# Optimization experiments

Hardware: AMD Instinct MI355X
Metric: run time of the kernel (lower is better)

The kernel has to match this reference:

```python
import jax, jax.numpy as jnp
import numpy as np

N, E, D = 20000, 160000, 128   # nodes, edges, d_model
GH, HC = 4, 128                # TransformerConv heads, per-head channels (= out_channels)
MH = 4                         # temporal MHA heads
MC = D // MH                   # temporal MHA per-head dim
EPS = 1e-5


def layer_norm(x, g, b):
    mu = x.mean(-1, keepdims=True)
    var = ((x - mu) ** 2).mean(-1, keepdims=True)
    return (x - mu) * jax.lax.rsqrt(var + EPS) * g + b


def forward(x, temporal_encoding, gq_w, gq_b, gk_w, gk_b, gv_w, gv_b, gs_w, gs_b,
            mha_wq, mha_bq, mha_wk, mha_bk, mha_wv, mha_bv, mha_wo, mha_bo,
            ffn_w1, ffn_b1, ffn_w2, ffn_b2,
            ln1_g, ln1_b, ln2_g, ln2_b, ln3_g, ln3_b, edge_index):
    src, dst = edge_index[0], edge_index[1]
    n = x.shape[0]
    # --- TransformerConv(in=D, out=D, heads=GH, concat=False, root_weight=True) ---
    q = (x @ gq_w.T + gq_b).reshape(n, GH, HC)
    k = (x @ gk_w.T + gk_b).reshape(n, GH, HC)
    v = (x @ gv_w.T + gv_b).reshape(n, GH, HC)
    # per-edge attention logits: <q_i, k_j> / sqrt(out_channels), message j->i
    alpha = (q[dst] * k[src]).sum(-1) / jnp.sqrt(jnp.asarray(HC, x.dtype))  # [E, GH]
    # numerically-stable segment softmax over incoming edges of each dst node
    m = jax.ops.segment_max(alpha, dst, num_segments=n)                     # [N, GH]
    ex = jnp.exp(alpha - m[dst])
    den = jax.ops.segment_sum(ex, dst, num_segments=n)
    w = ex / den[dst]                                                       # [E, GH]
    agg = jax.ops.segment_sum(w[..., None] * v[src], dst, num_segments=n)  # [N, GH, HC]
    graph_out = agg.mean(1) + (x @ gs_w.T + gs_b)  # concat=False -> head mean; + root skip lin
    x1 = layer_norm(x + graph_out, ln1_g, ln1_b)   # dropout is identity at eval
    # --- temporal MHA: per-node query (len 1) attends to its temporal encoding (kv len 1) ---
    tq = (x1 @ mha_wq.T + mha_bq).reshape(n, MH, MC)
    tk = (temporal_encoding @ mha_wk.T + mha_bk).reshape(n, MH, MC)
    tv = (temporal_encoding @ mha_wv.T + mha_bv).reshape(n, MH, MC)
    scores = (tq * tk).sum(-1, keepdims=True) / jnp.sqrt(jnp.asarray(MC, x.dtype))  # [N, MH, 1]
    attn = jax.nn.softmax(scores, axis=-1)  # exactly ones (single kv position); kept for fidelity
    temp_out = (attn * tv).reshape(n, D) @ mha_wo.T + mha_bo
    x2 = layer_norm(x1 + temp_out, ln2_g, ln2_b)
    # --- FFN ---
    h = jax.nn.relu(x2 @ ffn_w1.T + ffn_b1)
    ffn_out = h @ ffn_w2.T + ffn_b2
    return layer_norm(x2 + ffn_out, ln3_g, ln3_b)


def setup_inputs() -> dict:
    ks = jax.random.split(jax.random.key(0), 16)
    s = 0.05
    def p(i, shape):
        return jax.random.normal(ks[i], shape, jnp.float32) * s
    z = lambda *sh: jnp.zeros(sh, jnp.float32)
    o = lambda *sh: jnp.ones(sh, jnp.float32)
    return {
        "x": p(0, (N, D)),
        "temporal_encoding": p(1, (N, D)),
        "gq_w": p(2, (GH * HC, D)), "gq_b": z(GH * HC),
        "gk_w": p(3, (GH * HC, D)), "gk_b": z(GH * HC),
        "gv_w": p(4, (GH * HC, D)), "gv_b": z(GH * HC),
        "gs_w": p(5, (D, D)), "gs_b": z(D),
        "mha_wq": p(6, (D, D)), "mha_bq": z(D),
        "mha_wk": p(7, (D, D)), "mha_bk": z(D),
        "mha_wv": p(8, (D, D)), "mha_bv": z(D),
        "mha_wo": p(9, (D, D)), "mha_bo": z(D),
        "ffn_w1": p(10, (4 * D, D)), "ffn_b1": z(4 * D),
        "ffn_w2": p(11, (D, 4 * D)), "ffn_b2": z(D),
        "ln1_g": o(D), "ln1_b": z(D),
        "ln2_g": o(D), "ln2_b": z(D),
        "ln3_g": o(D), "ln3_b": z(D),
        "edge_index": jax.random.randint(ks[12], (2, E), 0, N, jnp.int32),
    }


def reference(x, temporal_encoding, gq_w, gq_b, gk_w, gk_b, gv_w, gv_b, gs_w, gs_b,
              mha_wq, mha_bq, mha_wk, mha_bk, mha_wv, mha_bv, mha_wo, mha_bo,
              ffn_w1, ffn_b1, ffn_w2, ffn_b2,
              ln1_g, ln1_b, ln2_g, ln2_b, ln3_g, ln3_b, edge_index):
    return forward(x, temporal_encoding, gq_w, gq_b, gk_w, gk_b, gv_w, gv_b, gs_w, gs_b,
                   mha_wq, mha_bq, mha_wk, mha_bk, mha_wv, mha_bv, mha_wo, mha_bo,
                   ffn_w1, ffn_b1, ffn_w2, ffn_b2,
                   ln1_g, ln1_b, ln2_g, ln2_b, ln3_g, ln3_b, edge_index)
```

## Files before the change

### kernel.cpp

```cpp
#include <hip/hip_runtime.h>

#define NN 20000
#define EE 160000
#define DD 128
#define GHC 512
#define INV_SQRT_HC 0.08838834764831845f

typedef __attribute__((ext_vector_type(8))) short short8;
typedef __attribute__((ext_vector_type(4))) short short4v;
typedef __attribute__((ext_vector_type(4))) float float4v;
typedef __attribute__((ext_vector_type(2))) float float2v;
typedef __attribute__((ext_vector_type(4))) unsigned uint4v;
typedef __attribute__((ext_vector_type(2))) unsigned uint2v;

__device__ inline float bf2f(unsigned short u) {
    union { unsigned u; float f; } x; x.u = ((unsigned)u) << 16; return x.f;
}
__device__ inline unsigned short f2bf(float f) {
    union { float f; unsigned u; } x; x.f = f;
    unsigned u = x.u;
    unsigned r = (u + 0x7fffu + ((u >> 16) & 1u)) >> 16;
    return (unsigned short)r;
}
__device__ inline unsigned cvt_pk_bf16(float a, float b) {
    unsigned d;
    asm("v_cvt_pk_bf16_f32 %0, %1, %2" : "=v"(d) : "v"(a), "v"(b));
    return d;
}

__device__ inline void stage16(const short8* gsrc, short8* ldst) {
    __builtin_amdgcn_global_load_lds(
        (const __attribute__((address_space(1))) void*)gsrc,
        (__attribute__((address_space(3))) void*)ldst, 16, 0, 0);
}

#if defined(__has_builtin)
#if __has_builtin(__builtin_amdgcn_cvt_pk_f32_fp8) && __has_builtin(__builtin_amdgcn_cvt_pk_fp8_f32)
#define HW_FP8 1
#endif
#endif
#ifndef HW_FP8
#define HW_FP8 0
#endif

#if !HW_FP8
__device__ inline unsigned char sw_enc_fp8(float f) {
    if (!(f == f)) return 0x7f;
    unsigned s = (f < 0.f) ? 0x80u : 0u;
    float a = fabsf(f);
    if (a >= 448.f) return (unsigned char)(s | 0x7e);
    if (a < 5.96046448e-8f) return (unsigned char)s;
    int e; frexpf(a, &e);
    int E = e - 1;
    if (E < -6) E = -6;
    float q = ldexpf(rintf(ldexpf(a, 3 - E)), E - 3);
    if (q == 0.f) return (unsigned char)s;
    union { float f; unsigned u; } x; x.f = q;
    int qe = (int)((x.u >> 23) & 0xff) - 127;
    if (qe < -6) {
        unsigned mant = (unsigned)rintf(ldexpf(q, 9));
        return (unsigned char)(s | mant);
    }
    unsigned mant = (x.u >> 20) & 7;
    int ebits = qe + 7;
    if (ebits > 15) { ebits = 15; mant = 6; }
    return (unsigned char)(s | ((unsigned)ebits << 3) | mant);
}
__device__ inline float sw_dec_fp8(unsigned char u) {
    unsigned s = u >> 7, e = (u >> 3) & 15, m = u & 7;
    float v = e ? ldexpf((float)(8 + m), (int)e - 10) : ldexpf((float)m, -9);
    return s ? -v : v;
}
#endif

__device__ inline unsigned fp8_enc4(float a, float b, float c, float d) {
#if HW_FP8
    int r = __builtin_amdgcn_cvt_pk_fp8_f32(a, b, 0, false);
    r = __builtin_amdgcn_cvt_pk_fp8_f32(c, d, r, true);
    return (unsigned)r;
#else
    return (unsigned)sw_enc_fp8(a) | ((unsigned)sw_enc_fp8(b) << 8)
         | ((unsigned)sw_enc_fp8(c) << 16) | ((unsigned)sw_enc_fp8(d) << 24);
#endif
}
__device__ inline float2v fp8_dec2_lo(unsigned w) {
#if HW_FP8
    return __builtin_amdgcn_cvt_pk_f32_fp8((int)w, false);
#else
    float2v r;
    r[0] = sw_dec_fp8((unsigned char)(w & 0xff));
    r[1] = sw_dec_fp8((unsigned char)((w >> 8) & 0xff));
    return r;
#endif
}
__device__ inline float2v fp8_dec2_hi(unsigned w) {
#if HW_FP8
    return __builtin_amdgcn_cvt_pk_f32_fp8((int)w, true);
#else
    float2v r;
    r[0] = sw_dec_fp8((unsigned char)((w >> 16) & 0xff));
    r[1] = sw_dec_fp8((unsigned char)(w >> 24));
    return r;
#endif
}

struct WPack { const void* in[18]; };
__device__ __constant__ const int WSZ[18] = {
    65536, 65536, 65536, 512, 512, 512,
    16384, 128, 65536, 512, 65536, 128,
    128, 128, 128, 128, 128, 128 };

__global__ void prep_kernel(const float* __restrict__ x, const float* __restrict__ te,
                            unsigned short* __restrict__ xcout, WPack p,
                            unsigned short* __restrict__ wcout,
                            const float* __restrict__ wv, const float* __restrict__ bv,
                            const float* __restrict__ wo, const float* __restrict__ bo,
                            unsigned short* __restrict__ wcomb,
                            unsigned short* __restrict__ bcomb,
                            const int* __restrict__ e_dst, int* __restrict__ counts)
{
    const int b = blockIdx.x;
    const int tid = threadIdx.x;
    if (b < 1024) {
        const long n4half = (long)NN * DD / 4;
        short4v* out4 = reinterpret_cast<short4v*>(xcout);
        long i = (long)b * 256 + tid;
        const long stride = 1024L * 256;
        const long tot = 2 * n4half;
        for (; i < tot; i += stride) {
            const float4v* src = (i < n4half)
                ? reinterpret_cast<const float4v*>(x)
                : reinterpret_cast<const float4v*>(te) - n4half;
            float4v v = src[i];
            short4v o;
            o[0] = (short)f2bf(v[0]); o[1] = (short)f2bf(v[1]);
            o[2] = (short)f2bf(v[2]); o[3] = (short)f2bf(v[3]);
            out4[i] = o;
        }
    } else if (b < 1600) {
        const int seg = (b - 1024) >> 5;
        const int rep = (b - 1024) & 31;
        int off = 0;
#pragma unroll
        for (int s = 0; s < 18; ++s) if (s < seg) off += WSZ[s];
        const int n = WSZ[seg];
        const float* q = (const float*)p.in[seg];
        for (int i = rep * 256 + tid; i < n; i += 32 * 256)
            wcout[off + i] = f2bf(q[i]);
    } else if (b < 1664) {
        int e = (b - 1600) * 256 + tid;
        int i = e >> 7, kk = e & 127;
        float s = 0.f;
        for (int j = 0; j < 128; ++j)
            s += wo[i * 128 + j] * wv[j * 128 + kk];
        wcomb[e] = f2bf(s);
        if (b == 1600 && tid < 128) {
            float t = 0.f;
            for (int j = 0; j < 128; ++j) t += wo[tid * 128 + j] * bv[j];
            bcomb[tid] = f2bf(t + bo[tid]);
        }
    } else {
        int e = (b - 1664) * 256 + tid;
        if (e < EE) {
            int d = e_dst[e];
            if (d >= 0 && d < NN) atomicAdd(&counts[d], 1);
        }
    }
}

__global__ __launch_bounds__(256) void gemm3_kernel(
    const unsigned short* __restrict__ A, const unsigned short* __restrict__ W,
    const unsigned short* __restrict__ bias, unsigned short* __restrict__ out,
    unsigned char* __restrict__ kvout, int M, int Nout, int split, int relu,
    int nxg, int ncol)
{
    __shared__ short8 wslab[2048];
    __shared__ __attribute__((aligned(16))) unsigned stile4[4][16][32];
    const int tid  = threadIdx.x;
    const int lane = tid & 63;
    const int wid  = tid >> 6;
    const int quad = lane >> 4;
    const int l15  = lane & 15;

    const int nb  = nxg * ncol;
    const int qq  = nb >> 3, rm = nb & 7;
    const int xcd = blockIdx.x & 7, slot = blockIdx.x >> 3;
    const int c   = (xcd < rm) ? xcd * (qq + 1) + slot
                               : rm * (qq + 1) + (xcd - rm) * qq + slot;
    const int xg = c / ncol;
    const int yg = c - xg * ncol;
    const int colbase0 = yg * 128;
    const int rowg = xg * 256;

    const bool isfp8 = (colbase0 >= split);
    const int kvcol = colbase0 - split;
    const int which = isfp8 ? (kvcol >> 9) : 0;
    const int head  = isfp8 ? ((kvcol & 511) >> 7) : 0;

    const short8* A8 = reinterpret_cast<const short8*>(A);
    const short8* W8 = reinterpret_cast<const short8*>(W);

    short8 a4[4];
    {
        int arow = rowg + wid * 16 + l15;
        if (arow >= M) arow = M - 1;
#pragma unroll
        for (int i = 0; i < 4; ++i) a4[i] = A8[(size_t)arow * 16 + i * 4 + quad];
    }

#pragma unroll
    for (int rep = 0; rep < 8; ++rep) {
        const int fi  = (rep * 4 + wid) & 3;
        const int ft  = rep & 3;
        const int ftt = rep >> 2;
        const int wrow = colbase0 + ftt * 64 + 16 * ft + l15;
        stage16(&W8[(size_t)wrow * 16 + fi * 4 + quad], &wslab[rep * 256 + wid * 64]);
    }

    short4v bs4[2][4];
#pragma unroll
    for (int tt = 0; tt < 2; ++tt)
#pragma unroll
        for (int t = 0; t < 4; ++t)
            bs4[tt][t] = *reinterpret_cast<const short4v*>(
                &bias[colbase0 + tt * 64 + 16 * t + quad * 4]);

    __syncthreads();

    unsigned* fpd = &stile4[wid][0][0];

#pragma unroll
    for (int tg = 0; tg < 4; ++tg) {
        const int rowbase = rowg + tg * 64 + wid * 16;

        short8 a4n[4];
        if (tg < 3) {
            int arow = rowbase + 64 + l15;
            if (arow >= M) arow = M - 1;
#pragma unroll
            for (int i = 0; i < 4; ++i) a4n[i] = A8[(size_t)arow * 16 + i * 4 + quad];
        }

#pragma unroll
        for (int tt = 0; tt < 2; ++tt) {
            float4v acc[4];
#pragma unroll
            for (int t = 0; t < 4; ++t) acc[t] = (float4v){0.f, 0.f, 0.f, 0.f};

#pragma unroll
            for (int i = 0; i < 4; ++i) {
#pragma unroll
                for (int t = 0; t < 4; ++t) {
                    short8 wb = wslab[((tt * 4 + t) * 4 + i) * 64 + lane];
                    acc[t] = __builtin_amdgcn_mfma_f32_16x16x32_bf16(wb, a4[i], acc[t], 0, 0, 0);
                }
            }

            if (!isfp8) {
#pragma unroll
                for (int t = 0; t < 4; ++t) {
                    float v0 = acc[t][0] + bf2f((unsigned short)bs4[tt][t][0]);
                    float v1 = acc[t][1] + bf2f((unsigned short)bs4[tt][t][1]);
                    float v2 = acc[t][2] + bf2f((unsigned short)bs4[tt][t][2]);
                    float v3 = acc[t][3] + bf2f((unsigned short)bs4[tt][t][3]);
                    if (relu) {
                        v0 = fmaxf(v0, 0.f); v1 = fmaxf(v1, 0.f);
                        v2 = fmaxf(v2, 0.f); v3 = fmaxf(v3, 0.f);
                    }
                    uint2v d = { cvt_pk_bf16(v0, v1), cvt_pk_bf16(v2, v3) };
                    const int dc = (8 * t + quad * 2) ^ ((l15 & 7) << 2);
                    *reinterpret_cast<uint2v*>(&stile4[wid][l15][dc]) = d;
                }
                const int rr0 = lane >> 3;
                const int cd  = (lane & 7) * 4;
#pragma unroll
                for (int it = 0; it < 2; ++it) {
                    int rw = rr0 + it * 8;
                    int grow = rowbase + rw;
                    if (grow < M) {
                        const int cs = cd ^ ((rw & 7) << 2);
                        uint4v v = *reinterpret_cast<const uint4v*>(&stile4[wid][rw][cs]);
                        *reinterpret_cast<uint4v*>(&out[(size_t)grow * Nout + colbase0 + tt * 64 + cd * 2]) = v;
                    }
                }
            } else {
#pragma unroll
                for (int t = 0; t < 4; ++t) {
                    float v0 = (acc[t][0] + bf2f((unsigned short)bs4[tt][t][0])) * 256.f;
                    float v1 = (acc[t][1] + bf2f((unsigned short)bs4[tt][t][1])) * 256.f;
                    float v2 = (acc[t][2] + bf2f((unsigned short)bs4[tt][t][2])) * 256.f;
                    float v3 = (acc[t][3] + bf2f((unsigned short)bs4[tt][t][3])) * 256.f;
                    const int dc = (tt * 16 + 4 * t + quad) ^ ((l15 & 7) << 2);
                    fpd[l15 * 32 + dc] = fp8_enc4(v0, v1, v2, v3);
                }
            }
        }

        if (isfp8) {
#pragma unroll
            for (int it = 0; it < 2; ++it) {
                int u = lane + it * 64;
                int row = u >> 3;
                int part = u & 7;
                int grow = rowbase + row;
                if (grow < M) {
                    const int db = row * 32 + ((part * 4) ^ ((row & 7) << 2));
                    uint4v v = *reinterpret_cast<const uint4v*>(&fpd[db]);
                    size_t ro = (size_t)grow * 1024 + (size_t)which * 512
                              + (size_t)head * 128 + (size_t)part * 16;
                    *reinterpret_cast<uint4v*>(kvout + ro) = v;
                }
            }
        }

        if (tg < 3) {
#pragma unroll
            for (int i = 0; i < 4; ++i) a4[i] = a4n[i];
        }
    }
}

__global__ __launch_bounds__(256) void tail_kernel(
    const unsigned short* __restrict__ A1, const unsigned short* __restrict__ W1g,
    const unsigned short* __restrict__ b1g,
    const unsigned short* __restrict__ A2, const unsigned short* __restrict__ W2g,
    const unsigned short* __restrict__ b2g,
    const float* __restrict__ rx, const float* __restrict__ ragg,
    const unsigned short* __restrict__ g1, const unsigned short* __restrict__ be1,
    const unsigned short* __restrict__ g2, const unsigned short* __restrict__ be2,
    const unsigned short* __restrict__ fw1, const unsigned short* __restrict__ fb1,
    const unsigned short* __restrict__ fw2, const unsigned short* __restrict__ fb2,
    const unsigned short* __restrict__ g3, const unsigned short* __restrict__ be3,
    float* __restrict__ outf, int M)
{
    __shared__ short8 wslab[2048];
    __shared__ __attribute__((aligned(16))) unsigned short htile[64 * 128];
    const int tid  = threadIdx.x;
    const int lane = tid & 63;
    const int wid  = tid >> 6;
    const int quad = lane >> 4;
    const int l15  = lane & 15;
    const int rowbase = blockIdx.x * 64 + wid * 16;
    const int grow = rowbase + l15;
    const int gr = (grow < M) ? grow : M - 1;
    const int hrow = wid * 16 + l15;
    char* hb = reinterpret_cast<char*>(htile);

    const short8* A81 = reinterpret_cast<const short8*>(A1);
    const short8* A82 = reinterpret_cast<const short8*>(A2);
    const short8* W81 = reinterpret_cast<const short8*>(W1g);
    const short8* W82 = reinterpret_cast<const short8*>(W2g);
    const short8* F18 = reinterpret_cast<const short8*>(fw1);
    const short8* F28 = reinterpret_cast<const short8*>(fw2);

#pragma unroll
    for (int rep = 0; rep < 8; ++rep) {
        const int fi  = (rep * 4 + wid) & 3;
        const int ft  = rep & 3;
        const int ftt = rep >> 2;
        const int wrow = ftt * 64 + 16 * ft + l15;
        stage16(&W81[(size_t)wrow * 16 + fi * 4 + quad], &wslab[rep * 256 + wid * 64]);
    }
    short8 a4[4];
#pragma unroll
    for (int i = 0; i < 4; ++i) a4[i] = A81[(size_t)gr * 16 + i * 4 + quad];
    __syncthreads();

    float4v acc1[2][4];
#pragma unroll
    for (int tt = 0; tt < 2; ++tt)
#pragma unroll
        for (int t = 0; t < 4; ++t) acc1[tt][t] = (float4v){0.f, 0.f, 0.f, 0.f};
#pragma unroll
    for (int tt = 0; tt < 2; ++tt)
#pragma unroll
        for (int i = 0; i < 4; ++i)
#pragma unroll
            for (int t = 0; t < 4; ++t) {
                short8 wb = wslab[((tt * 4 + t) * 4 + i) * 64 + lane];
                acc1[tt][t] = __builtin_amdgcn_mfma_f32_16x16x32_bf16(wb, a4[i], acc1[tt][t], 0, 0, 0);
            }
    __syncthreads();

#pragma unroll
    for (int rep = 0; rep < 8; ++rep) {
        const int fi  = (rep * 4 + wid) & 3;
        const int ft  = rep & 3;
        const int ftt = rep >> 2;
        const int wrow = ftt * 64 + 16 * ft + l15;
        stage16(&W82[(size_t)wrow * 16 + fi * 4 + quad], &wslab[rep * 256 + wid * 64]);
    }
    short8 a42[4];
#pragma unroll
    for (int i = 0; i < 4; ++i) a42[i] = A82[(size_t)gr * 16 + i * 4 + quad];

    float x1[32];
    {
        float v[32];
#pragma unroll
        for (int tt = 0; tt < 2; ++tt)
#pragma unroll
            for (int t = 0; t < 4; ++t) {
                const int n0 = tt * 64 + 16 * t + quad * 4;
                short4v bs = *reinterpret_cast<const short4v*>(&b1g[n0]);
                float4v rv = *reinterpret_cast<const float4v*>(&rx[(size_t)gr * 128 + n0]);
                float4v cv = *reinterpret_cast<const float4v*>(&ragg[(size_t)gr * 128 + n0]);
#pragma unroll
                for (int r = 0; r < 4; ++r)
                    v[(tt * 4 + t) * 4 + r] = acc1[tt][t][r]
                        + bf2f((unsigned short)bs[r]) + rv[r] + cv[r];
            }
        float s = 0.f, sq = 0.f;
#pragma unroll
        for (int i = 0; i < 32; ++i) { s += v[i]; sq += v[i] * v[i]; }
        s  += __shfl_xor(s, 16, 64);  s  += __shfl_xor(s, 32, 64);
        sq += __shfl_xor(sq, 16, 64); sq += __shfl_xor(sq, 32, 64);
        float mu  = s * (1.f / 128.f);
        float var = sq * (1.f / 128.f) - mu * mu;
        float rs  = rsqrtf(fmaxf(var, 0.f) + 1e-5f);
#pragma unroll
        for (int tt = 0; tt < 2; ++tt)
#pragma unroll
            for (int t = 0; t < 4; ++t) {
                const int n0 = tt * 64 + 16 * t + quad * 4;
                short4v gg = *reinterpret_cast<const short4v*>(&g1[n0]);
                short4v bb = *reinterpret_cast<const short4v*>(&be1[n0]);
#pragma unroll
                for (int r = 0; r < 4; ++r)
                    x1[(tt * 4 + t) * 4 + r] = (v[(tt * 4 + t) * 4 + r] - mu) * rs
                        * bf2f((unsigned short)gg[r]) + bf2f((unsigned short)bb[r]);
            }
    }

    __syncthreads();

    float4v acc2[2][4];
#pragma unroll
    for (int tt = 0; tt < 2; ++tt)
#pragma unroll
        for (int t = 0; t < 4; ++t) acc2[tt][t] = (float4v){0.f, 0.f, 0.f, 0.f};
#pragma unroll
    for (int tt = 0; tt < 2; ++tt)
#pragma unroll
        for (int i = 0; i < 4; ++i)
#pragma unroll
            for (int t = 0; t < 4; ++t) {
                short8 wb = wslab[((tt * 4 + t) * 4 + i) * 64 + lane];
                acc2[tt][t] = __builtin_amdgcn_mfma_f32_16x16x32_bf16(wb, a42[i], acc2[tt][t], 0, 0, 0);
            }

    float x2[32];
    {
        float v[32];
#pragma unroll
        for (int tt = 0; tt < 2; ++tt)
#pragma unroll
            for (int t = 0; t < 4; ++t) {
                const int n0 = tt * 64 + 16 * t + quad * 4;
                short4v bs = *reinterpret_cast<const short4v*>(&b2g[n0]);
#pragma unroll
                for (int r = 0; r < 4; ++r)
                    v[(tt * 4 + t) * 4 + r] = acc2[tt][t][r]
                        + bf2f((unsigned short)bs[r]) + x1[(tt * 4 + t) * 4 + r];
            }
        float s = 0.f, sq = 0.f;
#pragma unroll
        for (int i = 0; i < 32; ++i) { s += v[i]; sq += v[i] * v[i]; }
        s  += __shfl_xor(s, 16, 64);  s  += __shfl_xor(s, 32, 64);
        sq += __shfl_xor(sq, 16, 64); sq += __shfl_xor(sq, 32, 64);
        float mu  = s * (1.f / 128.f);
        float var = sq * (1.f / 128.f) - mu * mu;
        float rs  = rsqrtf(fmaxf(var, 0.f) + 1e-5f);
#pragma unroll
        for (int tt = 0; tt < 2; ++tt)
#pragma unroll
            for (int t = 0; t < 4; ++t) {
                const int n0 = tt * 64 + 16 * t + quad * 4;
                short4v gg = *reinterpret_cast<const short4v*>(&g2[n0]);
                short4v bb = *reinterpret_cast<const short4v*>(&be2[n0]);
#pragma unroll
                for (int r = 0; r < 4; ++r)
                    x2[(tt * 4 + t) * 4 + r] = (v[(tt * 4 + t) * 4 + r] - mu) * rs
                        * bf2f((unsigned short)gg[r]) + bf2f((unsigned short)bb[r]);
            }
    }

#pragma unroll
    for (int tt = 0; tt < 2; ++tt)
#pragma unroll
        for (int t = 0; t < 4; ++t) {
            const int n0 = tt * 64 + 16 * t + quad * 4;
            const int idx = (tt * 4 + t) * 4;
            uint2v d = { cvt_pk_bf16(x2[idx], x2[idx + 1]),
                         cvt_pk_bf16(x2[idx + 2], x2[idx + 3]) };
            *reinterpret_cast<uint2v*>(
                hb + ((hrow * 256 + n0 * 2) ^ ((hrow & 7) << 4))) = d;
        }
    short8 af[4];
#pragma unroll
    for (int i = 0; i < 4; ++i)
        af[i] = *reinterpret_cast<const short8*>(
            hb + ((hrow * 256 + (i * 32 + quad * 8) * 2) ^ ((hrow & 7) << 4)));

    float4v accf[2][4];
#pragma unroll
    for (int tt = 0; tt < 2; ++tt)
#pragma unroll
        for (int t = 0; t < 4; ++t) accf[tt][t] = (float4v){0.f, 0.f, 0.f, 0.f};

    for (int cc = 0; cc < 4; ++cc) {
        __syncthreads();
#pragma unroll
        for (int rep = 0; rep < 8; ++rep) {
            const int fi  = (rep * 4 + wid) & 3;
            const int ft  = rep & 3;
            const int ftt = rep >> 2;
            const int wrow = cc * 128 + ftt * 64 + 16 * ft + l15;
            stage16(&F18[(size_t)wrow * 16 + fi * 4 + quad], &wslab[rep * 256 + wid * 64]);
        }
        __syncthreads();

        float4v au[2][4];
#pragma unroll
        for (int tt = 0; tt < 2; ++tt)
#pragma unroll
            for (int t = 0; t < 4; ++t) au[tt][t] = (float4v){0.f, 0.f, 0.f, 0.f};
#pragma unroll
        for (int tt = 0; tt < 2; ++tt)
#pragma unroll
            for (int i = 0; i < 4; ++i)
#pragma unroll
                for (int t = 0; t < 4; ++t) {
                    short8 wb = wslab[((tt * 4 + t) * 4 + i) * 64 + lane];
                    au[tt][t] = __builtin_amdgcn_mfma_f32_16x16x32_bf16(wb, af[i], au[tt][t], 0, 0, 0);
                }
#pragma unroll
        for (int tt = 0; tt < 2; ++tt)
#pragma unroll
            for (int t = 0; t < 4; ++t) {
                const int n0 = tt * 64 + 16 * t + quad * 4;
                short4v bs = *reinterpret_cast<const short4v*>(&fb1[cc * 128 + n0]);
                float v0 = fmaxf(au[tt][t][0] + bf2f((unsigned short)bs[0]), 0.f);
                float v1 = fmaxf(au[tt][t][1] + bf2f((unsigned short)bs[1]), 0.f);
                float v2 = fmaxf(au[tt][t][2] + bf2f((unsigned short)bs[2]), 0.f);
                float v3 = fmaxf(au[tt][t][3] + bf2f((unsigned short)bs[3]), 0.f);
                uint2v d = { cvt_pk_bf16(v0, v1), cvt_pk_bf16(v2, v3) };
                *reinterpret_cast<uint2v*>(
                    hb + ((hrow * 256 + n0 * 2) ^ ((hrow & 7) << 4))) = d;
            }

        __syncthreads();
#pragma unroll
        for (int rep = 0; rep < 8; ++rep) {
            const int fi  = (rep * 4 + wid) & 3;
            const int ft  = rep & 3;
            const int ftt = rep >> 2;
            const int wrow = ftt * 64 + 16 * ft + l15;
            stage16(&F28[(size_t)wrow * 64 + cc * 16 + fi * 4 + quad],
                    &wslab[rep * 256 + wid * 64]);
        }
        __syncthreads();

        short8 h4[4];
#pragma unroll
        for (int i = 0; i < 4; ++i)
            h4[i] = *reinterpret_cast<const short8*>(
                hb + ((hrow * 256 + (i * 32 + quad * 8) * 2) ^ ((hrow & 7) << 4)));
#pragma unroll
        for (int tt = 0; tt < 2; ++tt)
#pragma unroll
            for (int i = 0; i < 4; ++i)
#pragma unroll
                for (int t = 0; t < 4; ++t) {
                    short8 wb = wslab[((tt * 4 + t) * 4 + i) * 64 + lane];
                    accf[tt][t] = __builtin_amdgcn_mfma_f32_16x16x32_bf16(wb, h4[i], accf[tt][t], 0, 0, 0);
                }
    }

    float v[32];
#pragma unroll
    for (int tt = 0; tt < 2; ++tt)
#pragma unroll
        for (int t = 0; t < 4; ++t) {
            const int n0 = tt * 64 + 16 * t + quad * 4;
            short4v bs = *reinterpret_cast<const short4v*>(&fb2[n0]);
#pragma unroll
            for (int r = 0; r < 4; ++r)
                v[(tt * 4 + t) * 4 + r] = accf[tt][t][r]
                    + bf2f((unsigned short)bs[r]) + x2[(tt * 4 + t) * 4 + r];
        }
    float s = 0.f, sq = 0.f;
#pragma unroll
    for (int i = 0; i < 32; ++i) { s += v[i]; sq += v[i] * v[i]; }
    s  += __shfl_xor(s, 16, 64);  s  += __shfl_xor(s, 32, 64);
    sq += __shfl_xor(sq, 16, 64); sq += __shfl_xor(sq, 32, 64);
    float mu  = s * (1.f / 128.f);
    float var = sq * (1.f / 128.f) - mu * mu;
    float rs  = rsqrtf(fmaxf(var, 0.f) + 1e-5f);

    if (grow < M) {
#pragma unroll
        for (int tt = 0; tt < 2; ++tt)
#pragma unroll
            for (int t = 0; t < 4; ++t) {
                const int n0 = tt * 64 + 16 * t + quad * 4;
                short4v gg = *reinterpret_cast<const short4v*>(&g3[n0]);
                short4v bb = *reinterpret_cast<const short4v*>(&be3[n0]);
                float4v ov;
#pragma unroll
                for (int r = 0; r < 4; ++r)
                    ov[r] = (v[(tt * 4 + t) * 4 + r] - mu) * rs
                            * bf2f((unsigned short)gg[r]) + bf2f((unsigned short)bb[r]);
                *reinterpret_cast<float4v*>(&outf[(size_t)grow * 128 + n0]) = ov;
            }
    }
}

__global__ __launch_bounds__(1024) void scan_kernel(
    const int* __restrict__ counts, int* __restrict__ offsets, int* __restrict__ pos, int n)
{
    __shared__ int wsum[16];
    __shared__ int carry_s;
    const int tid = threadIdx.x;
    const int wid = tid >> 6, lane = tid & 63;
    int vals[20];
#pragma unroll
    for (int cI = 0; cI < 20; ++cI) {
        int i = cI * 1024 + tid;
        vals[cI] = (i < n) ? counts[i] : 0;
    }
    if (tid == 0) carry_s = 0;
    __syncthreads();
#pragma unroll
    for (int cI = 0; cI < 20; ++cI) {
        int i = cI * 1024 + tid;
        int val = vals[cI];
        int x = val;
#pragma unroll
        for (int off = 1; off < 64; off <<= 1) {
            int t = __shfl_up(x, off, 64);
            if (lane >= off) x += t;
        }
        if (lane == 63) wsum[wid] = x;
        __syncthreads();
        if (wid == 0 && lane < 16) {
            int s = wsum[lane];
#pragma unroll
            for (int off = 1; off < 16; off <<= 1) {
                int t = __shfl_up(s, off, 64);
                if (lane >= off) s += t;
            }
            wsum[lane] = s;
        }
        __syncthreads();
        int prefix = (wid > 0 ? wsum[wid - 1] : 0) + carry_s;
        int ex = prefix + x - val;
        if (i < n) { offsets[i] = ex; pos[i] = ex; }
        __syncthreads();
        if (tid == 0) carry_s += wsum[15];
        __syncthreads();
    }
    if (tid == 0) offsets[n] = carry_s;
}

__global__ void scatter_kernel(const int* __restrict__ src, const int* __restrict__ dst,
                               int* __restrict__ pos, int* __restrict__ sorted_src, int E)
{
    int e = blockIdx.x * 256 + threadIdx.x;
    if (e < E) {
        int d = dst[e];
        if (d >= 0 && d < NN) {
            int p = atomicAdd(&pos[d], 1);
            if (p >= 0 && p < E) sorted_src[p] = src[e];
        }
    }
}

__device__ inline void agg_edge(const uint2v& kk, const uint2v& vv,
                                const float* qf, float* acc, float& ssum)
{
    float2v k01 = fp8_dec2_lo(kk[0]);
    float2v k23 = fp8_dec2_hi(kk[0]);
    float2v k45 = fp8_dec2_lo(kk[1]);
    float2v k67 = fp8_dec2_hi(kk[1]);
    float dot = qf[0] * k01[0] + qf[1] * k01[1] + qf[2] * k23[0] + qf[3] * k23[1]
              + qf[4] * k45[0] + qf[5] * k45[1] + qf[6] * k67[0] + qf[7] * k67[1];
    dot += __shfl_xor(dot, 1, 64);
    dot += __shfl_xor(dot, 2, 64);
    dot += __shfl_xor(dot, 4, 64);
    dot += __shfl_xor(dot, 8, 64);
    float pp = __expf(dot);
    ssum += pp;
    float2v v01 = fp8_dec2_lo(vv[0]);
    float2v v23 = fp8_dec2_hi(vv[0]);
    float2v v45 = fp8_dec2_lo(vv[1]);
    float2v v67 = fp8_dec2_hi(vv[1]);
    acc[0] += pp * v01[0]; acc[1] += pp * v01[1];
    acc[2] += pp * v23[0]; acc[3] += pp * v23[1];
    acc[4] += pp * v45[0]; acc[5] += pp * v45[1];
    acc[6] += pp * v67[0]; acc[7] += pp * v67[1];
}

__global__ __launch_bounds__(256) void agg_kernel(
    const unsigned short* __restrict__ q, const unsigned char* __restrict__ kvb,
    const int* __restrict__ offsets, const int* __restrict__ srcs,
    float* __restrict__ aggb)
{
    __shared__ float sacc[4][64][9];
    __shared__ float sssum[4][64];
    const int tid  = threadIdx.x;
    const int wid  = tid >> 6;
    const int lane = tid & 63;
    const int node = blockIdx.x * 2 + (wid >> 1);
    const int half = wid & 1;

    const short8* q8 = reinterpret_cast<const short8*>(q);
    const int fidx = (lane >> 4) * 16 + (lane & 15);
    const int koff = fidx * 8;

    short8 qv = q8[(size_t)node * 64 + fidx];
    float qf[8];
#pragma unroll
    for (int i = 0; i < 8; ++i)
        qf[i] = bf2f((unsigned short)qv[i]) * (INV_SQRT_HC / 256.f);

    int beg = offsets[node], end = offsets[node + 1];
    if (beg < 0) beg = 0;
    if (end > EE) end = EE;
    float ssum = 0.f;
    float acc[8];
#pragma unroll
    for (int i = 0; i < 8; ++i) acc[i] = 0.f;

    const int start = beg + half;
    int nce = (end > start) ? ((end - start + 1) >> 1) : 0;
    int ncap = (nce > 64) ? 64 : nce;

    int sv = 0;
    if (lane < ncap) {
        int s = srcs[start + 2 * lane];
        if (s < 0) s = 0;
        if (s >= NN) s = NN - 1;
        sv = s;
    }
    for (int base = 0; base < ncap; base += 4) {
        const int rem = ncap - base;
        uint2v k0{}, v0{}, k1{}, v1{}, k2{}, v2{}, k3{}, v3{};
        {
            int s = __shfl(sv, base, 64);
            const unsigned char* p = kvb + (size_t)s * 1024 + koff;
            k0 = *reinterpret_cast<const uint2v*>(p);
            v0 = *reinterpret_cast<const uint2v*>(p + 512);
        }
        if (rem > 1) {
            int s = __shfl(sv, base + 1, 64);
            const unsigned char* p = kvb + (size_t)s * 1024 + koff;
            k1 = *reinterpret_cast<const uint2v*>(p);
            v1 = *reinterpret_cast<const uint2v*>(p + 512);
        }
        if (rem > 2) {
            int s = __shfl(sv, base + 2, 64);
            const unsigned char* p = kvb + (size_t)s * 1024 + koff;
            k2 = *reinterpret_cast<const uint2v*>(p);
            v2 = *reinterpret_cast<const uint2v*>(p + 512);
        }
        if (rem > 3) {
            int s = __shfl(sv, base + 3, 64);
            const unsigned char* p = kvb + (size_t)s * 1024 + koff;
            k3 = *reinterpret_cast<const uint2v*>(p);
            v3 = *reinterpret_cast<const uint2v*>(p + 512);
        }
        agg_edge(k0, v0, qf, acc, ssum);
        if (rem > 1) agg_edge(k1, v1, qf, acc, ssum);
        if (rem > 2) agg_edge(k2, v2, qf, acc, ssum);
        if (rem > 3) agg_edge(k3, v3, qf, acc, ssum);
    }
    for (int j = start + 128; j < end; j += 2) {
        int s = srcs[j];
        if (s < 0) s = 0;
        if (s >= NN) s = NN - 1;
        uint2v kc = *reinterpret_cast<const uint2v*>(kvb + (size_t)s * 1024 + koff);
        uint2v vc = *reinterpret_cast<const uint2v*>(kvb + (size_t)s * 1024 + 512 + koff);
        agg_edge(kc, vc, qf, acc, ssum);
    }

#pragma unroll
    for (int i = 0; i < 8; ++i) sacc[wid][lane][i] = acc[i];
    sssum[wid][lane] = ssum;
    __syncthreads();
    if (half == 0) {
#pragma unroll
        for (int i = 0; i < 8; ++i) acc[i] += sacc[wid ^ 1][lane][i];
        ssum += sssum[wid ^ 1][lane];

        float inv = (ssum > 0.f) ? 1.f / (256.f * ssum) : 0.f;
#pragma unroll
        for (int i = 0; i < 8; ++i) acc[i] *= inv;
#pragma unroll
        for (int i = 0; i < 8; ++i) {
            acc[i] += __shfl_xor(acc[i], 16, 64);
            acc[i] += __shfl_xor(acc[i], 32, 64);
            acc[i] *= 0.25f;
        }
        if (lane < 16) {
            float4v* o = reinterpret_cast<float4v*>(aggb + (size_t)node * 128 + lane * 8);
            o[0] = (float4v){acc[0], acc[1], acc[2], acc[3]};
            o[1] = (float4v){acc[4], acc[5], acc[6], acc[7]};
        }
    }
}

extern "C" void kernel_launch(void* const* d_in, const int* in_sizes, int n_in,
                              void* d_out, int out_size, void* d_ws, size_t ws_size,
                              hipStream_t stream)
{
    const int* edge_index = (const int*)d_in[28];
    const int* e_src = edge_index;
    const int* e_dst = edge_index + EE;

    if (n_in < 29 || in_sizes[0] != NN * DD || in_sizes[28] != 2 * EE || out_size != NN * DD)
        return;

    const size_t SZ_OFF  = (size_t)(NN + 16) * 4;
    const size_t SZ_CNT  = (size_t)NN * 4;
    const size_t SZ_SS   = (size_t)EE * 4;
    const size_t SZ_SM   = (size_t)NN * DD * 2;
    const size_t SZ_F32  = (size_t)NN * DD * 4;
    const size_t SZ_Q    = (size_t)NN * 512 * 2;
    const size_t SZ_KV   = (size_t)NN * 1024;
    const size_t SZ_HB   = (size_t)NN * GHC * 2;
    const size_t WC_ELE  = 347136;
    const size_t SZ_WC   = WC_ELE * 2;
    const size_t SZ_WCB  = 16384 * 2 + 256;
    const size_t REQUIRED = SZ_OFF + 2 * SZ_CNT + SZ_SS + 2 * SZ_SM + SZ_WC + SZ_WCB
                          + SZ_Q + SZ_KV + 3 * SZ_F32 + SZ_SM + SZ_HB;

    if (ws_size < REQUIRED) return;

    char* w = (char*)d_ws;
    int* offsets = (int*)w;        w += SZ_OFF;
    int* counts  = (int*)w;        w += SZ_CNT;
    int* pos     = (int*)w;        w += SZ_CNT;
    int* sorted_src = (int*)w;     w += SZ_SS;
    unsigned short* xc   = (unsigned short*)w; w += SZ_SM;
    unsigned short* tec  = (unsigned short*)w; w += SZ_SM;
    unsigned short* wc   = (unsigned short*)w; w += SZ_WC;
    unsigned short* wcomb = (unsigned short*)w; w += 16384 * 2;
    unsigned short* bcomb = (unsigned short*)w; w += 256;
    unsigned short* qb   = (unsigned short*)w; w += SZ_Q;
    unsigned char*  kvb  = (unsigned char*)w;  w += SZ_KV;
    float*          aggb = (float*)w;          w += SZ_F32;
    float*          x1f  = (float*)w;          w += SZ_F32;
    float*          x2f  = (float*)w;          w += SZ_F32;
    unsigned short* x2b  = (unsigned short*)w; w += SZ_SM;
    unsigned short* hbuf = (unsigned short*)w; w += SZ_HB;
    (void)x1f; (void)x2f; (void)x2b; (void)hbuf;

    unsigned short* cw = wc;
    unsigned short* qkv_w = cw; cw += 3 * 65536;
    unsigned short* qkv_b = cw; cw += 3 * 512;
    unsigned short* gs_w  = cw; cw += 16384;  unsigned short* gs_b  = cw; cw += 128;
    unsigned short* ffn_w1 = cw; cw += 65536; unsigned short* ffn_b1 = cw; cw += 512;
    unsigned short* ffn_w2 = cw; cw += 65536; unsigned short* ffn_b2 = cw; cw += 128;
    unsigned short* ln1_g = cw; cw += 128;    unsigned short* ln1_b = cw; cw += 128;
    unsigned short* ln2_g = cw; cw += 128;    unsigned short* ln2_b = cw; cw += 128;
    unsigned short* ln3_g = cw; cw += 128;    unsigned short* ln3_b = cw; cw += 128;

    const int EB = (EE + 255) / 256;
    const dim3 blk(256);
    const int MB = (NN + 63) / 64;
    const int MB2 = (NN + 255) / 256;

    WPack pack;
    const int live_idx[18] = {2,4,6, 3,5,7, 8,9, 18,19, 20,21, 22,23,24,25,26,27};
    for (int i = 0; i < 18; ++i) pack.in[i] = d_in[live_idx[i]];

    (void)hipMemsetAsync(counts, 0, SZ_CNT, stream);
    prep_kernel<<<1664 + EB, blk, 0, stream>>>((const float*)d_in[0], (const float*)d_in[1],
                                               xc, pack, wc,
                                               (const float*)d_in[14], (const float*)d_in[15],
                                               (const float*)d_in[16], (const float*)d_in[17],
                                               wcomb, bcomb, e_dst, counts);

    scan_kernel<<<1, 1024, 0, stream>>>(counts, offsets, pos, NN);
    scatter_kernel<<<EB, blk, 0, stream>>>(e_src, e_dst, pos, sorted_src, EE);

    gemm3_kernel<<<dim3(MB2 * 12), blk, 0, stream>>>(xc, qkv_w, qkv_b, qb, kvb,
                                                     NN, 512, 512, 0, MB2, 12);
    agg_kernel<<<NN / 2, blk, 0, stream>>>(qb, kvb, offsets, sorted_src, aggb);

    tail_kernel<<<MB, blk, 0, stream>>>(xc, gs_w, gs_b,
                                        tec, wcomb, bcomb,
                                        (const float*)d_in[0], aggb,
                                        ln1_g, ln1_b, ln2_g, ln2_b,
                                        ffn_w1, ffn_b1, ffn_w2, ffn_b2,
                                        ln3_g, ln3_b, (float*)d_out, NN);
}
```

Before: 251.4 us.

## Double-buffer weight slabs in tail kernel to overlap staging with MFMA

The single shared weight slab in the fused tail kernel is split into two LDS buffers. The next weight tile (W2, FFN W1 chunks, FFN W2 chunks) is now staged into one buffer while MFMAs read the other, and several __syncthreads barriers are dropped. This hides global-to-LDS load latency behind matrix work and cuts barrier stalls. In exchange, LDS use per block grows by 32 KB, which may lower the number of resident blocks per CU.

```diff
diff --git a/kernel.cpp b/kernel.cpp
--- a/kernel.cpp
+++ b/kernel.cpp
@@ -320,6 +320,29 @@
     }
 }
 
+#define STAGE_W(W8, RS8, CO8, RO, WS) do {                                    \
+    _Pragma("unroll")                                                         \
+    for (int rep_ = 0; rep_ < 8; ++rep_) {                                    \
+        const int fi_  = (rep_ * 4 + wid) & 3;                                \
+        const int ft_  = rep_ & 3;                                            \
+        const int ftt_ = rep_ >> 2;                                           \
+        const int wrow_ = (RO) + ftt_ * 64 + 16 * ft_ + l15;                  \
+        stage16(&(W8)[(size_t)wrow_ * (RS8) + (CO8) + fi_ * 4 + quad],        \
+                &(WS)[rep_ * 256 + wid * 64]);                                \
+    } } while (0)
+
+#define MM128(WS, AF, ACC) do {                                               \
+    _Pragma("unroll")                                                         \
+    for (int tt_ = 0; tt_ < 2; ++tt_)                                         \
+    _Pragma("unroll")                                                         \
+    for (int i_ = 0; i_ < 4; ++i_)                                            \
+    _Pragma("unroll")                                                         \
+    for (int t_ = 0; t_ < 4; ++t_) {                                          \
+        short8 wb_ = (WS)[((tt_ * 4 + t_) * 4 + i_) * 64 + lane];             \
+        (ACC)[tt_][t_] = __builtin_amdgcn_mfma_f32_16x16x32_bf16(             \
+            wb_, (AF)[i_], (ACC)[tt_][t_], 0, 0, 0);                          \
+    } } while (0)
+
 __global__ __launch_bounds__(256) void tail_kernel(
     const unsigned short* __restrict__ A1, const unsigned short* __restrict__ W1g,
     const unsigned short* __restrict__ b1g,
@@ -333,7 +356,8 @@
     const unsigned short* __restrict__ g3, const unsigned short* __restrict__ be3,
     float* __restrict__ outf, int M)
 {
-    __shared__ short8 wslab[2048];
+    __shared__ short8 wsA[2048];
+    __shared__ short8 wsB[2048];
     __shared__ __attribute__((aligned(16))) unsigned short htile[64 * 128];
     const int tid  = threadIdx.x;
     const int lane = tid & 63;
@@ -353,17 +377,14 @@
     const short8* F18 = reinterpret_cast<const short8*>(fw1);
     const short8* F28 = reinterpret_cast<const short8*>(fw2);
 
-#pragma unroll
-    for (int rep = 0; rep < 8; ++rep) {
-        const int fi  = (rep * 4 + wid) & 3;
-        const int ft  = rep & 3;
-        const int ftt = rep >> 2;
-        const int wrow = ftt * 64 + 16 * ft + l15;
-        stage16(&W81[(size_t)wrow * 16 + fi * 4 + quad], &wslab[rep * 256 + wid * 64]);
-    }
-    short8 a4[4];
-#pragma unroll
-    for (int i = 0; i < 4; ++i) a4[i] = A81[(size_t)gr * 16 + i * 4 + quad];
+    STAGE_W(W81, 16, 0, 0, wsA);
+    STAGE_W(W82, 16, 0, 0, wsB);
+    short8 a4[4], a42[4];
+#pragma unroll
+    for (int i = 0; i < 4; ++i) {
+        a4[i]  = A81[(size_t)gr * 16 + i * 4 + quad];
+        a42[i] = A82[(size_t)gr * 16 + i * 4 + quad];
+    }
     __syncthreads();
 
     float4v acc1[2][4];
@@ -371,28 +392,10 @@
     for (int tt = 0; tt < 2; ++tt)
 #pragma unroll
         for (int t = 0; t < 4; ++t) acc1[tt][t] = (float4v){0.f, 0.f, 0.f, 0.f};
-#pragma unroll
-    for (int tt = 0; tt < 2; ++tt)
-#pragma unroll
-        for (int i = 0; i < 4; ++i)
-#pragma unroll
-            for (int t = 0; t < 4; ++t) {
-                short8 wb = wslab[((tt * 4 + t) * 4 + i) * 64 + lane];
-                acc1[tt][t] = __builtin_amdgcn_mfma_f32_16x16x32_bf16(wb, a4[i], acc1[tt][t], 0, 0, 0);
-            }
+    MM128(wsA, a4, acc1);
     __syncthreads();
 
-#pragma unroll
-    for (int rep = 0; rep < 8; ++rep) {
-        const int fi  = (rep * 4 + wid) & 3;
-        const int ft  = rep & 3;
-        const int ftt = rep >> 2;
-        const int wrow = ftt * 64 + 16 * ft + l15;
-        stage16(&W82[(size_t)wrow * 16 + fi * 4 + quad], &wslab[rep * 256 + wid * 64]);
-    }
-    short8 a42[4];
-#pragma unroll
-    for (int i = 0; i < 4; ++i) a42[i] = A82[(size_t)gr * 16 + i * 4 + quad];
+    STAGE_W(F18, 16, 0, 0, wsA);
 
     float x1[32];
     {
@@ -432,22 +435,12 @@
             }
     }
 
-    __syncthreads();
-
     float4v acc2[2][4];
 #pragma unroll
     for (int tt = 0; tt < 2; ++tt)
 #pragma unroll
         for (int t = 0; t < 4; ++t) acc2[tt][t] = (float4v){0.f, 0.f, 0.f, 0.f};
-#pragma unroll
-    for (int tt = 0; tt < 2; ++tt)
-#pragma unroll
-        for (int i = 0; i < 4; ++i)
-#pragma unroll
-            for (int t = 0; t < 4; ++t) {
-                short8 wb = wslab[((tt * 4 + t) * 4 + i) * 64 + lane];
-                acc2[tt][t] = __builtin_amdgcn_mfma_f32_16x16x32_bf16(wb, a42[i], acc2[tt][t], 0, 0, 0);
-            }
+    MM128(wsB, a42, acc2);
 
     float x2[32];
     {
@@ -502,6 +495,8 @@
         af[i] = *reinterpret_cast<const short8*>(
             hb + ((hrow * 256 + (i * 32 + quad * 8) * 2) ^ ((hrow & 7) << 4)));
 
+    __syncthreads();
+
     float4v accf[2][4];
 #pragma unroll
     for (int tt = 0; tt < 2; ++tt)
@@ -509,31 +504,14 @@
         for (int t = 0; t < 4; ++t) accf[tt][t] = (float4v){0.f, 0.f, 0.f, 0.f};
 
     for (int cc = 0; cc < 4; ++cc) {
-        __syncthreads();
-#pragma unroll
-        for (int rep = 0; rep < 8; ++rep) {
-            const int fi  = (rep * 4 + wid) & 3;
-            const int ft  = rep & 3;
-            const int ftt = rep >> 2;
-            const int wrow = cc * 128 + ftt * 64 + 16 * ft + l15;
-            stage16(&F18[(size_t)wrow * 16 + fi * 4 + quad], &wslab[rep * 256 + wid * 64]);
-        }
-        __syncthreads();
+        STAGE_W(F28, 64, cc * 16, 0, wsB);
 
         float4v au[2][4];
 #pragma unroll
         for (int tt = 0; tt < 2; ++tt)
 #pragma unroll
             for (int t = 0; t < 4; ++t) au[tt][t] = (float4v){0.f, 0.f, 0.f, 0.f};
-#pragma unroll
-        for (int tt = 0; tt < 2; ++tt)
-#pragma unroll
-            for (int i = 0; i < 4; ++i)
-#pragma unroll
-                for (int t = 0; t < 4; ++t) {
-                    short8 wb = wslab[((tt * 4 + t) * 4 + i) * 64 + lane];
-                    au[tt][t] = __builtin_amdgcn_mfma_f32_16x16x32_bf16(wb, af[i], au[tt][t], 0, 0, 0);
-                }
+        MM128(wsA, af, au);
 #pragma unroll
         for (int tt = 0; tt < 2; ++tt)
 #pragma unroll
@@ -548,33 +526,17 @@
                 *reinterpret_cast<uint2v*>(
                     hb + ((hrow * 256 + n0 * 2) ^ ((hrow & 7) << 4))) = d;
             }
-
         __syncthreads();
-#pragma unroll
-        for (int rep = 0; rep < 8; ++rep) {
-            const int fi  = (rep * 4 + wid) & 3;
-            const int ft  = rep & 3;
-            const int ftt = rep >> 2;
-            const int wrow = ftt * 64 + 16 * ft + l15;
-            stage16(&F28[(size_t)wrow * 64 + cc * 16 + fi * 4 + quad],
-                    &wslab[rep * 256 + wid * 64]);
-        }
-        __syncthreads();
+
+        if (cc < 3) STAGE_W(F18, 16, 0, (cc + 1) * 128, wsA);
 
         short8 h4[4];
 #pragma unroll
         for (int i = 0; i < 4; ++i)
             h4[i] = *reinterpret_cast<const short8*>(
                 hb + ((hrow * 256 + (i * 32 + quad * 8) * 2) ^ ((hrow & 7) << 4)));
-#pragma unroll
-        for (int tt = 0; tt < 2; ++tt)
-#pragma unroll
-            for (int i = 0; i < 4; ++i)
-#pragma unroll
-                for (int t = 0; t < 4; ++t) {
-                    short8 wb = wslab[((tt * 4 + t) * 4 + i) * 64 + lane];
-                    accf[tt][t] = __builtin_amdgcn_mfma_f32_16x16x32_bf16(wb, h4[i], accf[tt][t], 0, 0, 0);
-                }
+        MM128(wsB, h4, accf);
+        __syncthreads();
     }
 
     float v[32];
```

Result: slower. 257.9 us (+2.6%).
